# Kernel optimization log

Measured on AMD Instinct MI355X. Metric: run time of the kernel, lower is better.

## Reference

```python
import jax, jax.numpy as jnp
import numpy as np

TAG = 64
START = 0
END = 1
NEG = -10000.0


def setup_inputs() -> dict:
    key = jax.random.key(0)
    kf, kw, kl = jax.random.split(key, 3)
    B, T, K = 1024, 512, TAG
    feats = jax.random.normal(kf, (B, T, K), dtype=jnp.float32)
    w = jax.random.uniform(kw, (K, K), minval=-1.0 / K, maxval=1.0 / K, dtype=jnp.float32)
    # default adjacency: forbid transitions into start (row START) and out of end (col END)
    adj = jnp.zeros((K, K), jnp.float32).at[START, :].set(1.0).at[:, END].set(1.0)
    weights = w + NEG * adj
    lens = jax.random.randint(kl, (B,), 1, T + 1)  # 1..T inclusive
    return {"feats": feats, "weights": weights, "lens": lens}


def reference(feats, weights, lens):
    # feats: [B, T, K], weights: [K, K] with weights[next, prev], lens: [B]
    B, T, K = feats.shape
    init = jnp.full((B, K), NEG, feats.dtype).at[:, START].set(0.0)
    mask_tb = (jnp.arange(T)[None, :] < lens[:, None]).T  # [T, B]
    ident = jnp.arange(K, dtype=jnp.int32)

    def step(fv, inp):
        feat, m = inp  # feat: [B, K], m: [B]
        scores = fv[:, None, :] + weights[None, :, :]  # [B, next, prev]
        new_fv = jnp.max(scores, axis=-1) + feat       # emission added after max
        bptr = jnp.argmax(scores, axis=-1).astype(jnp.int32)
        fv2 = jnp.where(m[:, None], new_fv, fv)
        bptr2 = jnp.where(m[:, None], bptr, ident[None, :])  # identity keeps backtrace valid past len
        return fv2, bptr2

    fv, bptrs = jax.lax.scan(step, init, (jnp.swapaxes(feats, 0, 1), mask_tb))
    terminal = fv + weights[END][None, :]              # transition to end tag
    best_last = jnp.argmax(terminal, axis=-1)
    path_score = jnp.take_along_axis(terminal, best_last[:, None], axis=1)[:, 0]

    def back(tag, bp):  # tag: [B], bp: [B, K]
        prev = jnp.take_along_axis(bp, tag[:, None], axis=1)[:, 0]
        return prev, tag  # emit tag chosen at this timestep

    _, path = jax.lax.scan(back, best_last.astype(jnp.int32), bptrs, reverse=True)
    best_paths = jnp.swapaxes(path, 0, 1)  # [B, T]; positions >= lens[b] are padding
    return path_score, best_paths
```

## Files before the change

### kernel.cpp

```cpp
#include <hip/hip_runtime.h>

#define TAGS 64
#define MAXT 512
#define NEG  -10000.0f
#define CH   8

__global__ __launch_bounds__(64, 1) void crf_viterbi(
    const float* __restrict__ feats,
    const float* __restrict__ weights,
    const int*   __restrict__ lens,
    float*       __restrict__ out,
    int B, int T)
{
    const int b    = blockIdx.x;
    const int lane = threadIdx.x;
    const int len  = lens[b];

    __shared__ float fv[TAGS];
    __shared__ float fbuf[2][CH * TAGS];
    __shared__ unsigned char  bptr[MAXT * TAGS];
    __shared__ unsigned short path[MAXT];
    __shared__ float lds_pad[4608];

    if (b == 0x7fffffff) lds_pad[lane] = (float)len, fv[lane] = lds_pad[lane ^ 1];

    float4 w4[16];
    #pragma unroll
    for (int i = 0; i < 16; ++i)
        w4[i] = *reinterpret_cast<const float4*>(weights + lane * TAGS + i * 4);
    const float wEnd = weights[1 * TAGS + lane];

    fv[lane] = (lane == 0) ? 0.0f : NEG;

    const float* fb  = feats + (size_t)b * T * TAGS;
    const int    lim = len * TAGS - 4;

    float nf = NEG;

#define F3(a, b, c) fmaxf(fmaxf((a), (b)), (c))
#define M3(a, b, c) min(min((a), (b)), (c))

    auto step = [&](int cbuf, int i, int t) {
        const float feat = fbuf[cbuf][i * TAGS + lane];
        float4 fq[16];
        #pragma unroll
        for (int g = 0; g < 16; ++g)
            fq[g] = *reinterpret_cast<const float4*>(&fv[g * 4]);
        float4 c4[16];
        #pragma unroll
        for (int g = 0; g < 16; ++g) {
            c4[g].x = fq[g].x + w4[g].x;
            c4[g].y = fq[g].y + w4[g].y;
            c4[g].z = fq[g].z + w4[g].z;
            c4[g].w = fq[g].w + w4[g].w;
        }
        const float* c = reinterpret_cast<const float*>(c4);

        float v1[22];
        #pragma unroll
        for (int k = 0; k < 21; ++k) v1[k] = F3(c[3*k], c[3*k+1], c[3*k+2]);
        v1[21] = c[63];
        float v2[8];
        #pragma unroll
        for (int k = 0; k < 7; ++k) v2[k] = F3(v1[3*k], v1[3*k+1], v1[3*k+2]);
        v2[7] = v1[21];
        const float v30 = F3(v2[0], v2[1], v2[2]);
        const float v31 = F3(v2[3], v2[4], v2[5]);
        const float v32 = fmaxf(v2[6], v2[7]);
        const float m   = F3(v30, v31, v32);

        nf = m + feat;
        fv[lane] = nf;

        unsigned e[64];
        #pragma unroll
        for (int p = 0; p < 64; ++p) e[p] = (c[p] == m) ? (unsigned)p : 64u;
        unsigned u1[22];
        #pragma unroll
        for (int k = 0; k < 21; ++k) u1[k] = M3(e[3*k], e[3*k+1], e[3*k+2]);
        u1[21] = e[63];
        unsigned u2[8];
        #pragma unroll
        for (int k = 0; k < 7; ++k) u2[k] = M3(u1[3*k], u1[3*k+1], u1[3*k+2]);
        u2[7] = u1[21];
        const unsigned u30 = M3(u2[0], u2[1], u2[2]);
        const unsigned u31 = M3(u2[3], u2[4], u2[5]);
        const unsigned u32 = min(u2[6], u2[7]);
        const unsigned idx = M3(u30, u31, u32);

        bptr[t * TAGS + lane] = (unsigned char)idx;
    };

    {
        int o0 = 4 * lane;        if (o0 > lim) o0 = lim;
        int o1 = 256 + 4 * lane;  if (o1 > lim) o1 = lim;
        *reinterpret_cast<float4*>(&fbuf[0][4 * lane])       = *reinterpret_cast<const float4*>(fb + o0);
        *reinterpret_cast<float4*>(&fbuf[0][256 + 4 * lane]) = *reinterpret_cast<const float4*>(fb + o1);
    }
    float4 n0, n1;
    {
        int o0 = CH * TAGS + 4 * lane;        if (o0 > lim) o0 = lim;
        int o1 = CH * TAGS + 256 + 4 * lane;  if (o1 > lim) o1 = lim;
        n0 = *reinterpret_cast<const float4*>(fb + o0);
        n1 = *reinterpret_cast<const float4*>(fb + o1);
    }

    int cb = 0;
    const int nfull = len / CH;
    for (int c = 0; c < nfull; ++c) {
        #pragma unroll
        for (int i = 0; i < CH; ++i) step(cb, i, c * CH + i);
        *reinterpret_cast<float4*>(&fbuf[cb ^ 1][4 * lane])       = n0;
        *reinterpret_cast<float4*>(&fbuf[cb ^ 1][256 + 4 * lane]) = n1;
        {
            int o0 = (c + 2) * CH * TAGS + 4 * lane;        if (o0 > lim) o0 = lim;
            int o1 = (c + 2) * CH * TAGS + 256 + 4 * lane;  if (o1 > lim) o1 = lim;
            n0 = *reinterpret_cast<const float4*>(fb + o0);
            n1 = *reinterpret_cast<const float4*>(fb + o1);
        }
        cb ^= 1;
    }
    const int rem = len - nfull * CH;
    for (int i = 0; i < rem; ++i) step(cb, i, nfull * CH + i);

    float tv = nf + wEnd;
    int   ti = lane;
    #pragma unroll
    for (int off = 32; off >= 1; off >>= 1) {
        const float ov = __shfl_xor(tv, off);
        const int   oi = __shfl_xor(ti, off);
        if (ov > tv || (ov == tv && oi < ti)) { tv = ov; ti = oi; }
    }
    if (lane == 0) out[b] = tv;
    const int bestlast = ti;

    for (int t = lane; t < T; t += 64)
        if (t >= len - 1) path[t] = (unsigned short)bestlast;
    __builtin_amdgcn_wave_barrier();

    if (lane == 0) {
        int tag = bestlast;
        for (int t = len - 1; t >= 1; --t) {
            tag = bptr[t * TAGS + tag];
            path[t - 1] = (unsigned short)tag;
        }
    }
    __builtin_amdgcn_wave_barrier();

    float* pout = out + B + (size_t)b * T;
    for (int t = lane; t < T; t += 64)
        pout[t] = (float)path[t];
}

extern "C" void kernel_launch(void* const* d_in, const int* in_sizes, int n_in,
                              void* d_out, int out_size, void* d_ws, size_t ws_size,
                              hipStream_t stream) {
    const float* feats   = (const float*)d_in[0];
    const float* weights = (const float*)d_in[1];
    const int*   lens    = (const int*)d_in[2];
    float*       out     = (float*)d_out;

    const int B = in_sizes[2];
    const int T = in_sizes[0] / (B * TAGS);

    crf_viterbi<<<dim3(B), dim3(64), 0, stream>>>(feats, weights, lens, out, B, T);
}
```

Measured before the change: 426.5 us.

## Broadcast forward scores with readlane and keep features in registers

```diff
diff --git a/kernel.cpp b/kernel.cpp
--- a/kernel.cpp
+++ b/kernel.cpp
@@ -16,45 +16,33 @@
     const int lane = threadIdx.x;
     const int len  = lens[b];
 
-    __shared__ float fv[TAGS];
-    __shared__ float fbuf[2][CH * TAGS];
     __shared__ unsigned char  bptr[MAXT * TAGS];
     __shared__ unsigned short path[MAXT];
-    __shared__ float lds_pad[4608];
 
-    if (b == 0x7fffffff) lds_pad[lane] = (float)len, fv[lane] = lds_pad[lane ^ 1];
-
-    float4 w4[16];
+    float wf[TAGS];
     #pragma unroll
-    for (int i = 0; i < 16; ++i)
-        w4[i] = *reinterpret_cast<const float4*>(weights + lane * TAGS + i * 4);
+    for (int i = 0; i < 16; ++i) {
+        const float4 q = *reinterpret_cast<const float4*>(weights + lane * TAGS + i * 4);
+        wf[4*i+0] = q.x; wf[4*i+1] = q.y; wf[4*i+2] = q.z; wf[4*i+3] = q.w;
+    }
     const float wEnd = weights[1 * TAGS + lane];
 
-    fv[lane] = (lane == 0) ? 0.0f : NEG;
+    const float* fb  = feats + (size_t)b * T * TAGS;
+    const int    cap = len * TAGS;
 
-    const float* fb  = feats + (size_t)b * T * TAGS;
-    const int    lim = len * TAGS - 4;
-
-    float nf = NEG;
+    float nf = (lane == 0) ? 0.0f : NEG;
 
 #define F3(a, b, c) fmaxf(fmaxf((a), (b)), (c))
 #define M3(a, b, c) min(min((a), (b)), (c))
 
-    auto step = [&](int cbuf, int i, int t) {
-        const float feat = fbuf[cbuf][i * TAGS + lane];
-        float4 fq[16];
+    auto step = [&](float feat, int t) {
+        float c[64];
         #pragma unroll
-        for (int g = 0; g < 16; ++g)
-            fq[g] = *reinterpret_cast<const float4*>(&fv[g * 4]);
-        float4 c4[16];
-        #pragma unroll
-        for (int g = 0; g < 16; ++g) {
-            c4[g].x = fq[g].x + w4[g].x;
-            c4[g].y = fq[g].y + w4[g].y;
-            c4[g].z = fq[g].z + w4[g].z;
-            c4[g].w = fq[g].w + w4[g].w;
+        for (int p = 0; p < 64; ++p) {
+            const float fvp = __uint_as_float(
+                __builtin_amdgcn_readlane(__float_as_uint(nf), p));
+            c[p] = fvp + wf[p];
         }
-        const float* c = reinterpret_cast<const float*>(c4);
 
         float v1[22];
         #pragma unroll
@@ -70,7 +58,6 @@
         const float m   = F3(v30, v31, v32);
 
         nf = m + feat;
-        fv[lane] = nf;
 
         unsigned e[64];
         #pragma unroll
@@ -91,37 +78,34 @@
         bptr[t * TAGS + lane] = (unsigned char)idx;
     };
 
-    {
-        int o0 = 4 * lane;        if (o0 > lim) o0 = lim;
-        int o1 = 256 + 4 * lane;  if (o1 > lim) o1 = lim;
-        *reinterpret_cast<float4*>(&fbuf[0][4 * lane])       = *reinterpret_cast<const float4*>(fb + o0);
-        *reinterpret_cast<float4*>(&fbuf[0][256 + 4 * lane]) = *reinterpret_cast<const float4*>(fb + o1);
+    float fcur[CH], fnx[CH];
+    #pragma unroll
+    for (int i = 0; i < CH; ++i) {
+        int o = i * TAGS + lane; if (o >= cap) o = lane;
+        fcur[i] = fb[o];
     }
-    float4 n0, n1;
-    {
-        int o0 = CH * TAGS + 4 * lane;        if (o0 > lim) o0 = lim;
-        int o1 = CH * TAGS + 256 + 4 * lane;  if (o1 > lim) o1 = lim;
-        n0 = *reinterpret_cast<const float4*>(fb + o0);
-        n1 = *reinterpret_cast<const float4*>(fb + o1);
+    #pragma unroll
+    for (int i = 0; i < CH; ++i) {
+        int o = (CH + i) * TAGS + lane; if (o >= cap) o = lane;
+        fnx[i] = fb[o];
     }
 
-    int cb = 0;
     const int nfull = len / CH;
-    for (int c = 0; c < nfull; ++c) {
+    for (int ch = 0; ch < nfull; ++ch) {
         #pragma unroll
-        for (int i = 0; i < CH; ++i) step(cb, i, c * CH + i);
-        *reinterpret_cast<float4*>(&fbuf[cb ^ 1][4 * lane])       = n0;
-        *reinterpret_cast<float4*>(&fbuf[cb ^ 1][256 + 4 * lane]) = n1;
-        {
-            int o0 = (c + 2) * CH * TAGS + 4 * lane;        if (o0 > lim) o0 = lim;
-            int o1 = (c + 2) * CH * TAGS + 256 + 4 * lane;  if (o1 > lim) o1 = lim;
-            n0 = *reinterpret_cast<const float4*>(fb + o0);
-            n1 = *reinterpret_cast<const float4*>(fb + o1);
+        for (int i = 0; i < CH; ++i) step(fcur[i], ch * CH + i);
+        #pragma unroll
+        for (int i = 0; i < CH; ++i) fcur[i] = fnx[i];
+        #pragma unroll
+        for (int i = 0; i < CH; ++i) {
+            int o = (ch + 2) * CH * TAGS + i * TAGS + lane; if (o >= cap) o = lane;
+            fnx[i] = fb[o];
         }
-        cb ^= 1;
     }
     const int rem = len - nfull * CH;
-    for (int i = 0; i < rem; ++i) step(cb, i, nfull * CH + i);
+    #pragma unroll
+    for (int i = 0; i < CH; ++i)
+        if (i < rem) step(fcur[i], nfull * CH + i);
 
     float tv = nf + wEnd;
     int   ti = lane;
```

Measured after the change: 441.5 us. 3.5% more time.
